# Kernel optimization log

Hardware: AMD Instinct MI355X
Metric: run time of the kernel (lower is better)

The kernel has to match this reference:

```python
import jax, jax.numpy as jnp
import numpy as np

TEMPERATURE = 0.2
EPS = 1e-12

def _l2norm(x):
    # F.normalize(dim=1): x / max(||x||, eps)
    n = jnp.sqrt(jnp.sum(x * x, axis=1, keepdims=True))
    return x / jnp.maximum(n, EPS)

def setup_inputs() -> dict:
    key = jax.random.key(0)
    k1, k2, k3 = jax.random.split(key, 3)
    B, D, Q = 1024, 128, 65536
    return {
        "global_features_1": jax.random.normal(k1, (B, D), dtype=jnp.float32),
        "global_features_2": jax.random.normal(k2, (B, D), dtype=jnp.float32),
        "queue": jax.random.normal(k3, (Q, D), dtype=jnp.float32),
    }

def reference(global_features_1, global_features_2, queue):
    q = _l2norm(global_features_1)                    # [B, D]
    k = _l2norm(global_features_2)                    # [B, D]
    pos_sim = jnp.sum(q * k, axis=1, keepdims=True) / TEMPERATURE   # [B, 1]
    # queue renormalized under no_grad in the original
    queue_n = jax.lax.stop_gradient(_l2norm(queue))   # [Q, D]
    neg_sim = jnp.einsum('bd,qd->bq', q, queue_n) / TEMPERATURE     # [B, Q]
    logits = jnp.concatenate([pos_sim, neg_sim], axis=1)            # [B, 1+Q]
    # cross-entropy with label 0 for every row: -log_softmax(logits)[:, 0]
    log_probs = jax.nn.log_softmax(logits, axis=1)
    loss = -jnp.mean(log_probs[:, 0])
    return (loss, pos_sim, neg_sim)
```

## Files before the change

kernel.cpp:

```cpp
#include <hip/hip_runtime.h>
#include <math.h>

constexpr int B = 1024;
constexpr int D = 128;
constexpr int Q = 65536;
constexpr int NPART = 1024;
#define TEMP_INV 5.0f
#define EPS 1e-12f

typedef __bf16 bf16x8 __attribute__((ext_vector_type(8)));
typedef float  f32x4  __attribute__((ext_vector_type(4)));

__device__ __forceinline__ float wave_reduce_sum(float v) {
    #pragma unroll
    for (int off = 32; off > 0; off >>= 1) v += __shfl_xor(v, off);
    return v;
}

__device__ __forceinline__ unsigned short f2bf(float x) {
    unsigned int u = __float_as_uint(x);
    unsigned int r = (u + 0x7FFFu + ((u >> 16) & 1u)) >> 16;
    return (unsigned short)r;
}

__global__ __launch_bounds__(256) void k_prep(const float* __restrict__ g1,
                                              const float* __restrict__ g2,
                                              const float* __restrict__ queue,
                                              unsigned short* __restrict__ qnb,
                                              unsigned short* __restrict__ qb,
                                              float* __restrict__ out_pos,
                                              float* __restrict__ ws_pos) {
    if (blockIdx.x < Q / 8) {
        int half = threadIdx.x >> 5;
        int l    = threadIdx.x & 31;
        int row  = blockIdx.x * 8 + half;
        const f32x4* src = (const f32x4*)(queue + (size_t)row * D);
        f32x4 v = __builtin_nontemporal_load(&src[l]);
        float ss = v.x * v.x + v.y * v.y + v.z * v.z + v.w * v.w;
        #pragma unroll
        for (int off = 16; off > 0; off >>= 1) ss += __shfl_xor(ss, off);
        float inv = 1.0f / fmaxf(sqrtf(ss), EPS);
        uint2 o;
        o.x = (unsigned int)f2bf(v.x * inv) | ((unsigned int)f2bf(v.y * inv) << 16);
        o.y = (unsigned int)f2bf(v.z * inv) | ((unsigned int)f2bf(v.w * inv) << 16);
        ((uint2*)(qb + (size_t)row * D))[l] = o;
    } else {
        int idx = blockIdx.x - Q / 8;
        int w2 = threadIdx.x >> 7;
        int tt = threadIdx.x & 127;
        int b  = idx * 2 + w2;
        int w  = tt >> 6, lane = tt & 63;
        float x = g1[b * D + tt];
        float y = g2[b * D + tt];
        __shared__ float sx[2][2], sy[2][2], sp[2][2];
        float xs = wave_reduce_sum(x * x);
        float ys = wave_reduce_sum(y * y);
        if (lane == 0) { sx[w2][w] = xs; sy[w2][w] = ys; }
        __syncthreads();
        float ix = 1.0f / fmaxf(sqrtf(sx[w2][0] + sx[w2][1]), EPS);
        float iy = 1.0f / fmaxf(sqrtf(sy[w2][0] + sy[w2][1]), EPS);
        float qv = x * ix;
        float kv = y * iy;
        qnb[b * D + tt] = f2bf(qv);
        float p = wave_reduce_sum(qv * kv);
        if (lane == 0) sp[w2][w] = p;
        __syncthreads();
        if (tt == 0) {
            float pos = (sp[w2][0] + sp[w2][1]) * TEMP_INV;
            out_pos[b] = pos;
            ws_pos[b]  = pos;
        }
    }
}

__global__ __launch_bounds__(1024) void k_gemm_mfma(const unsigned short* __restrict__ qnb,
                                                    const unsigned short* __restrict__ qb,
                                                    float* __restrict__ neg,
                                                    float* __restrict__ psum) {
    __shared__ unsigned short SM[2][256][72];
    const int t  = threadIdx.x;
    const int blk = blockIdx.x;
    const int bx = blk >> 2;
    const int by = blk & 3;
    const int R0 = by * 256, C0 = bx * 256;
    const int wid = t >> 6, lane = t & 63;
    const int wr = wid >> 2, wc = wid & 3;
    const int lg = lane >> 4, lc = lane & 15;

    f32x4 acc[4][4];
    #pragma unroll
    for (int n = 0; n < 4; ++n)
        #pragma unroll
        for (int m = 0; m < 4; ++m)
            #pragma unroll
            for (int r = 0; r < 4; ++r) acc[n][m][r] = 0.0f;

    #pragma unroll
    for (int s = 0; s < 2; ++s) {
        if (s) __syncthreads();
        const int ks = s * 64;
        #pragma unroll
        for (int p = 0; p < 2; ++p) {
            int c   = t + 1024 * p;
            int row = c >> 3;
            int off = (c & 7) * 8;
            uint4 va = *(const uint4*)(qnb + (size_t)(R0 + row) * D + ks + off);
            uint4 vb = *(const uint4*)(qb  + (size_t)(C0 + row) * D + ks + off);
            *(uint4*)&SM[0][row][off] = va;
            *(uint4*)&SM[1][row][off] = vb;
        }
        __syncthreads();
        #pragma unroll
        for (int kk = 0; kk < 64; kk += 32) {
            int ko = kk + lg * 8;
            bf16x8 a[4], b[4];
            #pragma unroll
            for (int m = 0; m < 4; ++m)
                a[m] = *(const bf16x8*)&SM[0][wr * 64 + m * 16 + lc][ko];
            #pragma unroll
            for (int n = 0; n < 4; ++n)
                b[n] = *(const bf16x8*)&SM[1][wc * 64 + n * 16 + lc][ko];
            #pragma unroll
            for (int n = 0; n < 4; ++n)
                #pragma unroll
                for (int m = 0; m < 4; ++m)
                    acc[n][m] = __builtin_amdgcn_mfma_f32_16x16x32_bf16(b[n], a[m], acc[n][m], 0, 0, 0);
        }
    }

    const int slot = bx * 4 + wc;
    #pragma unroll
    for (int m = 0; m < 4; ++m) {
        const size_t rowBase = (size_t)(R0 + wr * 64 + m * 16 + lc) * Q + C0 + wc * 64;
        float e = 0.0f;
        #pragma unroll
        for (int n = 0; n < 4; ++n) {
            float v0 = acc[n][m][0] * TEMP_INV;
            float v1 = acc[n][m][1] * TEMP_INV;
            float v2 = acc[n][m][2] * TEMP_INV;
            float v3 = acc[n][m][3] * TEMP_INV;
            float4 o = make_float4(v0, v1, v2, v3);
            *(float4*)(neg + rowBase + n * 16 + lg * 4) = o;
            e += __expf(v0 - 5.0f) + __expf(v1 - 5.0f) +
                 __expf(v2 - 5.0f) + __expf(v3 - 5.0f);
        }
        e += __shfl_xor(e, 16);
        e += __shfl_xor(e, 32);
        if (lg == 0) {
            int gr = R0 + wr * 64 + m * 16 + lc;
            psum[(size_t)gr * NPART + slot] = e;
        }
    }
}

__global__ __launch_bounds__(256) void k_reduce_lse(const float* __restrict__ psum,
                                                    const float* __restrict__ ws_pos,
                                                    float* __restrict__ loss_b) {
    int r = blockIdx.x;
    const float4* pr = (const float4*)(psum + (size_t)r * NPART);
    float4 v = pr[threadIdx.x];
    float s = v.x + v.y + v.z + v.w;
    s = wave_reduce_sum(s);
    __shared__ float sw[4];
    int w = threadIdx.x >> 6, lane = threadIdx.x & 63;
    if (lane == 0) sw[w] = s;
    __syncthreads();
    if (threadIdx.x == 0) {
        float S = sw[0] + sw[1] + sw[2] + sw[3];
        float pos = ws_pos[r];
        S += __expf(pos - 5.0f);
        loss_b[r] = (logf(S) + 5.0f) - pos;
    }
}

__global__ void k_loss_mean(const float* __restrict__ loss_b, float* __restrict__ out) {
    float s = 0.0f;
    for (int i = threadIdx.x; i < B; i += 256) s += loss_b[i];
    s = wave_reduce_sum(s);
    __shared__ float sw[4];
    int w = threadIdx.x >> 6, lane = threadIdx.x & 63;
    if (lane == 0) sw[w] = s;
    __syncthreads();
    if (threadIdx.x == 0) out[0] = (sw[0] + sw[1] + sw[2] + sw[3]) / (float)B;
}

extern "C" void kernel_launch(void* const* d_in, const int* in_sizes, int n_in,
                              void* d_out, int out_size, void* d_ws, size_t ws_size,
                              hipStream_t stream) {
    const float* g1    = (const float*)d_in[0];
    const float* g2    = (const float*)d_in[1];
    const float* queue = (const float*)d_in[2];
    float* out = (float*)d_out;

    float* out_pos = out + 1;
    float* neg     = out + 1 + B;

    unsigned short* qnb = (unsigned short*)d_ws;
    unsigned short* qb  = qnb + (size_t)B * D;
    float* psum   = (float*)(qb + (size_t)Q * D);
    float* ws_pos = psum + (size_t)B * NPART;
    float* loss_b = ws_pos + B;

    k_prep<<<Q / 8 + B / 2, 256, 0, stream>>>(g1, g2, queue, qnb, qb, out_pos, ws_pos);
    k_gemm_mfma<<<(Q / 256) * (B / 256), 1024, 0, stream>>>(qnb, qb, neg, psum);
    k_reduce_lse<<<B, 256, 0, stream>>>(psum, ws_pos, loss_b);
    k_loss_mean<<<1, 256, 0, stream>>>(loss_b, out);
}
```

Baseline: 91.77 us.

## Fuse queue normalization into GEMM and keep queue tile resident across batch chunks

Queue rows are now normalized and converted to bf16 directly into shared memory inside the GEMM kernel, so the bf16 queue copy is no longer written to and reread from global memory. Each block keeps one 256-column queue tile resident and loops over four 256-row chunks of the batch, using the full K=128 per chunk. The separate loss-mean kernel is replaced by an atomicAdd into the output after a memset. The trade-off is fewer blocks (256 instead of 1024) with larger shared memory, which lowers occupancy and parallelism, and the loss sum order becomes nondeterministic.

```diff
diff --git a/kernel.cpp b/kernel.cpp
--- a/kernel.cpp
+++ b/kernel.cpp
@@ -17,145 +17,148 @@
     return v;
 }
 
-__device__ __forceinline__ unsigned short f2bf(float x) {
+__device__ __forceinline__ unsigned int f2bf(float x) {
     unsigned int u = __float_as_uint(x);
-    unsigned int r = (u + 0x7FFFu + ((u >> 16) & 1u)) >> 16;
-    return (unsigned short)r;
+    return (u + 0x7FFFu + ((u >> 16) & 1u)) >> 16;
 }
 
 __global__ __launch_bounds__(256) void k_prep(const float* __restrict__ g1,
                                               const float* __restrict__ g2,
-                                              const float* __restrict__ queue,
                                               unsigned short* __restrict__ qnb,
-                                              unsigned short* __restrict__ qb,
                                               float* __restrict__ out_pos,
                                               float* __restrict__ ws_pos) {
-    if (blockIdx.x < Q / 8) {
-        int half = threadIdx.x >> 5;
-        int l    = threadIdx.x & 31;
-        int row  = blockIdx.x * 8 + half;
-        const f32x4* src = (const f32x4*)(queue + (size_t)row * D);
-        f32x4 v = __builtin_nontemporal_load(&src[l]);
-        float ss = v.x * v.x + v.y * v.y + v.z * v.z + v.w * v.w;
-        #pragma unroll
-        for (int off = 16; off > 0; off >>= 1) ss += __shfl_xor(ss, off);
-        float inv = 1.0f / fmaxf(sqrtf(ss), EPS);
-        uint2 o;
-        o.x = (unsigned int)f2bf(v.x * inv) | ((unsigned int)f2bf(v.y * inv) << 16);
-        o.y = (unsigned int)f2bf(v.z * inv) | ((unsigned int)f2bf(v.w * inv) << 16);
-        ((uint2*)(qb + (size_t)row * D))[l] = o;
-    } else {
-        int idx = blockIdx.x - Q / 8;
-        int w2 = threadIdx.x >> 7;
-        int tt = threadIdx.x & 127;
-        int b  = idx * 2 + w2;
-        int w  = tt >> 6, lane = tt & 63;
-        float x = g1[b * D + tt];
-        float y = g2[b * D + tt];
-        __shared__ float sx[2][2], sy[2][2], sp[2][2];
-        float xs = wave_reduce_sum(x * x);
-        float ys = wave_reduce_sum(y * y);
-        if (lane == 0) { sx[w2][w] = xs; sy[w2][w] = ys; }
-        __syncthreads();
-        float ix = 1.0f / fmaxf(sqrtf(sx[w2][0] + sx[w2][1]), EPS);
-        float iy = 1.0f / fmaxf(sqrtf(sy[w2][0] + sy[w2][1]), EPS);
-        float qv = x * ix;
-        float kv = y * iy;
-        qnb[b * D + tt] = f2bf(qv);
-        float p = wave_reduce_sum(qv * kv);
-        if (lane == 0) sp[w2][w] = p;
-        __syncthreads();
-        if (tt == 0) {
-            float pos = (sp[w2][0] + sp[w2][1]) * TEMP_INV;
-            out_pos[b] = pos;
-            ws_pos[b]  = pos;
-        }
+    int w2 = threadIdx.x >> 7;
+    int tt = threadIdx.x & 127;
+    int b  = blockIdx.x * 2 + w2;
+    int w  = tt >> 6, lane = tt & 63;
+    float x = g1[b * D + tt];
+    float y = g2[b * D + tt];
+    __shared__ float sx[2][2], sy[2][2], sp[2][2];
+    float xs = wave_reduce_sum(x * x);
+    float ys = wave_reduce_sum(y * y);
+    if (lane == 0) { sx[w2][w] = xs; sy[w2][w] = ys; }
+    __syncthreads();
+    float ix = 1.0f / fmaxf(sqrtf(sx[w2][0] + sx[w2][1]), EPS);
+    float iy = 1.0f / fmaxf(sqrtf(sy[w2][0] + sy[w2][1]), EPS);
+    float qv = x * ix;
+    float kv = y * iy;
+    qnb[b * D + tt] = (unsigned short)f2bf(qv);
+    float p = wave_reduce_sum(qv * kv);
+    if (lane == 0) sp[w2][w] = p;
+    __syncthreads();
+    if (tt == 0) {
+        float pos = (sp[w2][0] + sp[w2][1]) * TEMP_INV;
+        out_pos[b] = pos;
+        ws_pos[b]  = pos;
     }
 }
 
-__global__ __launch_bounds__(1024) void k_gemm_mfma(const unsigned short* __restrict__ qnb,
-                                                    const unsigned short* __restrict__ qb,
-                                                    float* __restrict__ neg,
-                                                    float* __restrict__ psum) {
-    __shared__ unsigned short SM[2][256][72];
+__global__ __launch_bounds__(1024) void k_gemm_fused(const unsigned short* __restrict__ qnb,
+                                                     const float* __restrict__ queue,
+                                                     float* __restrict__ neg,
+                                                     float* __restrict__ psum) {
+    __shared__ unsigned short As[256][136];
+    __shared__ unsigned short Bs[256][136];
     const int t  = threadIdx.x;
-    const int blk = blockIdx.x;
-    const int bx = blk >> 2;
-    const int by = blk & 3;
-    const int R0 = by * 256, C0 = bx * 256;
+    const int bxn = blockIdx.x;
+    const int C0 = bxn * 256;
     const int wid = t >> 6, lane = t & 63;
     const int wr = wid >> 2, wc = wid & 3;
     const int lg = lane >> 4, lc = lane & 15;
 
-    f32x4 acc[4][4];
-    #pragma unroll
-    for (int n = 0; n < 4; ++n)
+    {
+        int row = t >> 2;
+        int seg = t & 3;
+        const f32x4* src = (const f32x4*)(queue + (size_t)(C0 + row) * D + seg * 32);
+        f32x4 u[8];
+        float ss = 0.0f;
         #pragma unroll
-        for (int m = 0; m < 4; ++m)
+        for (int i = 0; i < 8; ++i) {
+            u[i] = __builtin_nontemporal_load(src + i);
+            ss += u[i].x * u[i].x + u[i].y * u[i].y + u[i].z * u[i].z + u[i].w * u[i].w;
+        }
+        ss += __shfl_xor(ss, 1);
+        ss += __shfl_xor(ss, 2);
+        float inv = 1.0f / fmaxf(sqrtf(ss), EPS);
+        unsigned short* brow = &Bs[row][seg * 32];
+        #pragma unroll
+        for (int i = 0; i < 8; i += 2) {
+            uint4 wv;
+            wv.x = f2bf(u[i].x * inv)     | (f2bf(u[i].y * inv) << 16);
+            wv.y = f2bf(u[i].z * inv)     | (f2bf(u[i].w * inv) << 16);
+            wv.z = f2bf(u[i + 1].x * inv) | (f2bf(u[i + 1].y * inv) << 16);
+            wv.w = f2bf(u[i + 1].z * inv) | (f2bf(u[i + 1].w * inv) << 16);
+            *(uint4*)(brow + (i / 2) * 8) = wv;
+        }
+    }
+
+    for (int ch = 0; ch < 4; ++ch) {
+        __syncthreads();
+        {
+            int row = t >> 2;
+            int seg = t & 3;
+            const uint4* asrc = (const uint4*)(qnb + (size_t)(ch * 256 + row) * D + seg * 32);
+            unsigned short* arow = &As[row][seg * 32];
             #pragma unroll
-            for (int r = 0; r < 4; ++r) acc[n][m][r] = 0.0f;
-
-    #pragma unroll
-    for (int s = 0; s < 2; ++s) {
-        if (s) __syncthreads();
-        const int ks = s * 64;
-        #pragma unroll
-        for (int p = 0; p < 2; ++p) {
-            int c   = t + 1024 * p;
-            int row = c >> 3;
-            int off = (c & 7) * 8;
-            uint4 va = *(const uint4*)(qnb + (size_t)(R0 + row) * D + ks + off);
-            uint4 vb = *(const uint4*)(qb  + (size_t)(C0 + row) * D + ks + off);
-            *(uint4*)&SM[0][row][off] = va;
-            *(uint4*)&SM[1][row][off] = vb;
+            for (int j = 0; j < 4; ++j) *(uint4*)(arow + j * 8) = asrc[j];
         }
         __syncthreads();
+
+        f32x4 acc[4][4];
         #pragma unroll
-        for (int kk = 0; kk < 64; kk += 32) {
+        for (int n = 0; n < 4; ++n)
+            #pragma unroll
+            for (int m = 0; m < 4; ++m)
+                #pragma unroll
+                for (int r = 0; r < 4; ++r) acc[n][m][r] = 0.0f;
+
+        #pragma unroll
+        for (int kk = 0; kk < 128; kk += 32) {
             int ko = kk + lg * 8;
             bf16x8 a[4], b[4];
             #pragma unroll
             for (int m = 0; m < 4; ++m)
-                a[m] = *(const bf16x8*)&SM[0][wr * 64 + m * 16 + lc][ko];
+                a[m] = *(const bf16x8*)&As[wr * 64 + m * 16 + lc][ko];
             #pragma unroll
             for (int n = 0; n < 4; ++n)
-                b[n] = *(const bf16x8*)&SM[1][wc * 64 + n * 16 + lc][ko];
+                b[n] = *(const bf16x8*)&Bs[wc * 64 + n * 16 + lc][ko];
             #pragma unroll
             for (int n = 0; n < 4; ++n)
                 #pragma unroll
                 for (int m = 0; m < 4; ++m)
                     acc[n][m] = __builtin_amdgcn_mfma_f32_16x16x32_bf16(b[n], a[m], acc[n][m], 0, 0, 0);
         }
-    }
 
-    const int slot = bx * 4 + wc;
-    #pragma unroll
-    for (int m = 0; m < 4; ++m) {
-        const size_t rowBase = (size_t)(R0 + wr * 64 + m * 16 + lc) * Q + C0 + wc * 64;
-        float e = 0.0f;
+        const int R0 = ch * 256;
+        const int slot = bxn * 4 + wc;
         #pragma unroll
-        for (int n = 0; n < 4; ++n) {
-            float v0 = acc[n][m][0] * TEMP_INV;
-            float v1 = acc[n][m][1] * TEMP_INV;
-            float v2 = acc[n][m][2] * TEMP_INV;
-            float v3 = acc[n][m][3] * TEMP_INV;
-            float4 o = make_float4(v0, v1, v2, v3);
-            *(float4*)(neg + rowBase + n * 16 + lg * 4) = o;
-            e += __expf(v0 - 5.0f) + __expf(v1 - 5.0f) +
-                 __expf(v2 - 5.0f) + __expf(v3 - 5.0f);
-        }
-        e += __shfl_xor(e, 16);
-        e += __shfl_xor(e, 32);
-        if (lg == 0) {
-            int gr = R0 + wr * 64 + m * 16 + lc;
-            psum[(size_t)gr * NPART + slot] = e;
+        for (int m = 0; m < 4; ++m) {
+            const size_t rowBase = (size_t)(R0 + wr * 64 + m * 16 + lc) * Q + C0 + wc * 64;
+            float e = 0.0f;
+            #pragma unroll
+            for (int n = 0; n < 4; ++n) {
+                float v0 = acc[n][m][0] * TEMP_INV;
+                float v1 = acc[n][m][1] * TEMP_INV;
+                float v2 = acc[n][m][2] * TEMP_INV;
+                float v3 = acc[n][m][3] * TEMP_INV;
+                float4 o = make_float4(v0, v1, v2, v3);
+                *(float4*)(neg + rowBase + n * 16 + lg * 4) = o;
+                e += __expf(v0 - 5.0f) + __expf(v1 - 5.0f) +
+                     __expf(v2 - 5.0f) + __expf(v3 - 5.0f);
+            }
+            e += __shfl_xor(e, 16);
+            e += __shfl_xor(e, 32);
+            if (lg == 0) {
+                int gr = R0 + wr * 64 + m * 16 + lc;
+                psum[(size_t)gr * NPART + slot] = e;
+            }
         }
     }
 }
 
 __global__ __launch_bounds__(256) void k_reduce_lse(const float* __restrict__ psum,
                                                     const float* __restrict__ ws_pos,
-                                                    float* __restrict__ loss_b) {
+                                                    float* __restrict__ out) {
     int r = blockIdx.x;
     const float4* pr = (const float4*)(psum + (size_t)r * NPART);
     float4 v = pr[threadIdx.x];
@@ -169,19 +172,9 @@
         float S = sw[0] + sw[1] + sw[2] + sw[3];
         float pos = ws_pos[r];
         S += __expf(pos - 5.0f);
-        loss_b[r] = (logf(S) + 5.0f) - pos;
+        float loss = (logf(S) + 5.0f) - pos;
+        atomicAdd(out, loss * (1.0f / (float)B));
     }
-}
-
-__global__ void k_loss_mean(const float* __restrict__ loss_b, float* __restrict__ out) {
-    float s = 0.0f;
-    for (int i = threadIdx.x; i < B; i += 256) s += loss_b[i];
-    s = wave_reduce_sum(s);
-    __shared__ float sw[4];
-    int w = threadIdx.x >> 6, lane = threadIdx.x & 63;
-    if (lane == 0) sw[w] = s;
-    __syncthreads();
-    if (threadIdx.x == 0) out[0] = (sw[0] + sw[1] + sw[2] + sw[3]) / (float)B;
 }
 
 extern "C" void kernel_launch(void* const* d_in, const int* in_sizes, int n_in,
@@ -196,13 +189,11 @@
     float* neg     = out + 1 + B;
 
     unsigned short* qnb = (unsigned short*)d_ws;
-    unsigned short* qb  = qnb + (size_t)B * D;
-    float* psum   = (float*)(qb + (size_t)Q * D);
+    float* psum   = (float*)(qnb + (size_t)B * D);
     float* ws_pos = psum + (size_t)B * NPART;
-    float* loss_b = ws_pos + B;
 
-    k_prep<<<Q / 8 + B / 2, 256, 0, stream>>>(g1, g2, queue, qnb, qb, out_pos, ws_pos);
-    k_gemm_mfma<<<(Q / 256) * (B / 256), 1024, 0, stream>>>(qnb, qb, neg, psum);
-    k_reduce_lse<<<B, 256, 0, stream>>>(psum, ws_pos, loss_b);
-    k_loss_mean<<<1, 256, 0, stream>>>(loss_b, out);
+    hipMemsetAsync(out, 0, sizeof(float), stream);
+    k_prep<<<B / 2, 256, 0, stream>>>(g1, g2, qnb, out_pos, ws_pos);
+    k_gemm_fused<<<Q / 256, 1024, 0, stream>>>(qnb, queue, neg, psum);
+    k_reduce_lse<<<B, 256, 0, stream>>>(psum, ws_pos, out);
 }
```

After: 118.1 us. +28.7%, slower.
